# Performance work log

Hardware: AMD Instinct MI355X
Metric: run time of the kernel (lower is better)

The kernel has to match this reference:

```python
import jax, jax.numpy as jnp
import numpy as np

D_MODEL = 1024
BULK_DIM = 10          # int(log2(d_model))
ADS_RADIUS = 1.0
B, N = 4, 2048


def setup_inputs() -> dict:
    key = jax.random.key(0)
    k1, k2 = jax.random.split(key, 2)
    boundary_tokens = jax.random.normal(k1, (B, N, D_MODEL), dtype=jnp.float32)
    W_b2b = jax.random.normal(k2, (D_MODEL, D_MODEL * BULK_DIM), dtype=jnp.float32) / np.sqrt(D_MODEL).astype(np.float32)
    b_b2b = jnp.zeros((D_MODEL * BULK_DIM,), dtype=jnp.float32)
    return {"boundary_tokens": boundary_tokens, "W_b2b": W_b2b, "b_b2b": b_b2b}


def _fast_marching(bulk_coords, ads_radius):
    # bulk_coords: (B, N, K, D). Sequential eikonal-style sweep through the
    # bulk depth z = 1..K; AdS warp factor L/z attenuates the front update
    # deeper into the bulk. Returns geodesics with the same shape.
    cz = jnp.moveaxis(bulk_coords, 2, 0)                 # (K, B, N, D)
    z = jnp.arange(1, bulk_coords.shape[2] + 1, dtype=bulk_coords.dtype)
    factors = ads_radius / z                             # (K,)

    def step(g, inp):
        c, f = inp
        g_new = g + f * (c - g)
        return g_new, g_new

    _, geos = jax.lax.scan(step, cz[0], (cz, factors))   # (K, B, N, D)
    return jnp.moveaxis(geos, 0, 2)                      # (B, N, K, D)


def reference(boundary_tokens, W_b2b, b_b2b):
    Bb, Nn, D = boundary_tokens.shape
    # boundary -> bulk linear projection, reshaped to (B, N, bulk_dim, D)
    bulk_coords = (boundary_tokens @ W_b2b + b_b2b).reshape(Bb, Nn, BULK_DIM, D)
    geodesics = _fast_marching(bulk_coords, ADS_RADIUS)  # (B, N, K, D)
    bulk_features = geodesics.mean(axis=2)               # (B, N, D)
    return bulk_features
```

## Files before the change

### kernel.cpp

```cpp
#include <hip/hip_runtime.h>
#include <stdint.h>


static constexpr float FW[10] = {
    0.2928968253968254f, 0.1928968253968254f, 0.1428968253968254f,
    0.1095634920634921f, 0.0845634920634921f, 0.0645634920634921f,
    0.0478968253968254f, 0.0336111111111111f, 0.0211111111111111f,
    0.0100000000000000f};

typedef __attribute__((ext_vector_type(8))) short short8;
typedef __attribute__((ext_vector_type(4))) float floatx4;
typedef __attribute__((ext_vector_type(16))) float floatx16;

__device__ inline unsigned int bf16pack2(float hi, float lo) {
    unsigned int uh = __float_as_uint(hi) + 0x8000u;
    unsigned int ul = __float_as_uint(lo) + 0x8000u;
    return __builtin_amdgcn_perm(uh, ul, 0x07060302u);
}

#define LDS_AS(p) ((__attribute__((address_space(3))) unsigned int*)(p))
#define GLB_AS(p) ((const __attribute__((address_space(1))) unsigned int*)(p))

__global__ __launch_bounds__(256) void prep(const float* __restrict__ W,
                                            const float* __restrict__ tokens,
                                            const float* __restrict__ b,
                                            unsigned short* __restrict__ Wt,
                                            float* __restrict__ beff,
                                            uint4* __restrict__ Ab,
                                            int do_cvt) {
    __shared__ float T[32 * 65];
    const int t = threadIdx.x;
    const int bid = blockIdx.x;

    if (bid < 512) {
        const int n0 = (bid & 15) * 64;
        const int k0 = (bid >> 4) * 32;
#pragma unroll
        for (int s = 0; s < 2; ++s) {
            int slot = s * 256 + t;
            int r = slot >> 4;
            int c4 = (slot & 15) * 4;
            const float4* src = (const float4*)(W + (size_t)(k0 + r) * 10240 + n0 + c4);
            float4 acc = {0.f, 0.f, 0.f, 0.f};
#pragma unroll
            for (int j = 0; j < 10; ++j) {
                float4 v = src[j * 256];
                acc.x += FW[j] * v.x; acc.y += FW[j] * v.y;
                acc.z += FW[j] * v.z; acc.w += FW[j] * v.w;
            }
            T[r * 65 + c4 + 0] = acc.x;
            T[r * 65 + c4 + 1] = acc.y;
            T[r * 65 + c4 + 2] = acc.z;
            T[r * 65 + c4 + 3] = acc.w;
        }
        __syncthreads();
#pragma unroll
        for (int s = 0; s < 2; ++s) {
            int slot = s * 256 + t;
            int nl = slot >> 3;
            int k4 = (slot & 7) * 4;
            float f0 = T[(k4 + 0) * 65 + nl];
            float f1 = T[(k4 + 1) * 65 + nl];
            float f2 = T[(k4 + 2) * 65 + nl];
            float f3 = T[(k4 + 3) * 65 + nl];
            uint2 p;
            p.x = bf16pack2(f1, f0);
            p.y = bf16pack2(f3, f2);
            *(uint2*)(Wt + (size_t)(n0 + nl) * 1024 + k0 + k4) = p;
        }
        return;
    }
    if (bid == 512) {
        const float4* src = (const float4*)b + t;
        float4 acc = {0.f, 0.f, 0.f, 0.f};
#pragma unroll
        for (int j = 0; j < 10; ++j) {
            float4 v = src[j * 256];
            acc.x += FW[j] * v.x; acc.y += FW[j] * v.y;
            acc.z += FW[j] * v.z; acc.w += FW[j] * v.w;
        }
        ((float4*)beff)[t] = acc;
        return;
    }
    if (do_cvt) {
        size_t i = (size_t)(bid - 513) * 256 + t;
        const float4* src = (const float4*)tokens + i * 2;
        float4 a0 = src[0], a1 = src[1];
        uint4 p;
        p.x = bf16pack2(a0.y, a0.x);
        p.y = bf16pack2(a0.w, a0.z);
        p.z = bf16pack2(a1.y, a1.x);
        p.w = bf16pack2(a1.w, a1.z);
        Ab[i] = p;
    }
}

__global__ __launch_bounds__(256) void gemm32(const unsigned short* __restrict__ Ab,
                                              const unsigned short* __restrict__ Wt,
                                              const float* __restrict__ beff,
                                              float* __restrict__ C) {
    __shared__ __align__(16) unsigned char As[4][8192];
    __shared__ __align__(16) unsigned char Bs[4][8192];

    const int t = threadIdx.x;
    const int lane = t & 63;
    const int w = t >> 6;
    const int l31 = lane & 31;
    const int khalf = lane >> 5;
    const int wm = (w & 1) * 64;
    const int wn = (w >> 1) * 64;
    const int bm = blockIdx.x * 128;
    const int bn = blockIdx.y * 128;

    floatx16 acc[2][2];
#pragma unroll
    for (int i = 0; i < 2; ++i)
#pragma unroll
        for (int j = 0; j < 2; ++j)
#pragma unroll
            for (int r = 0; r < 16; ++r) acc[i][j][r] = 0.f;

    const char* Abase = (const char*)Ab + (size_t)bm * 2048;
    const char* Bbase = (const char*)Wt + (size_t)bn * 2048;

    int sm[2], sc[2];
#pragma unroll
    for (int i = 0; i < 2; ++i) {
        int s = (w * 2 + i) * 64 + lane;
        int pair = s >> 3;
        int q = (s & 7) ^ (pair & 7);
        sm[i] = pair * 2 + (q & 1);
        sc[i] = q >> 1;
    }

#define STAGE(KT)                                                                     \
    {                                                                                 \
        const size_t koff = (size_t)(KT) * 64;                                        \
        unsigned char* Ad = As[(KT) & 3];                                             \
        unsigned char* Bd = Bs[(KT) & 3];                                             \
        _Pragma("unroll") for (int i = 0; i < 2; ++i) {                               \
            int I = w * 2 + i;                                                        \
            __builtin_amdgcn_global_load_lds(                                         \
                GLB_AS(Abase + (size_t)sm[i] * 2048 + koff + sc[i] * 16),             \
                LDS_AS(Ad + I * 1024), 16, 0, 0);                                     \
            __builtin_amdgcn_global_load_lds(                                         \
                GLB_AS(Bbase + (size_t)sm[i] * 2048 + koff + sc[i] * 16),             \
                LDS_AS(Bd + I * 1024), 16, 0, 0);                                     \
        }                                                                             \
    }

    STAGE(0)
    STAGE(1)
    STAGE(2)

#pragma unroll
    for (int kt = 0; kt < 32; ++kt) {
        if (kt < 30)
            asm volatile("s_waitcnt vmcnt(8)" ::: "memory");
        else if (kt == 30)
            asm volatile("s_waitcnt vmcnt(4)" ::: "memory");
        else
            asm volatile("s_waitcnt vmcnt(0)" ::: "memory");
        __builtin_amdgcn_s_barrier();
        __builtin_amdgcn_sched_barrier(0);

        if (kt < 29) STAGE(kt + 3)
        __builtin_amdgcn_sched_barrier(0);

        const unsigned char* Acur = As[kt & 3];
        const unsigned char* Bcur = Bs[kt & 3];
#pragma unroll
        for (int kk = 0; kk < 2; ++kk) {
            int f = kk * 2 + khalf;
            short8 af[2], bf[2];
#pragma unroll
            for (int tm = 0; tm < 2; ++tm) {
                int m = wm + tm * 32 + l31;
                int slot = (m >> 1) * 8 + ((2 * f + (m & 1)) ^ ((m >> 1) & 7));
                af[tm] = *(const short8*)(Acur + slot * 16);
            }
#pragma unroll
            for (int tn = 0; tn < 2; ++tn) {
                int n = wn + tn * 32 + l31;
                int slot = (n >> 1) * 8 + ((2 * f + (n & 1)) ^ ((n >> 1) & 7));
                bf[tn] = *(const short8*)(Bcur + slot * 16);
            }
#pragma unroll
            for (int tm = 0; tm < 2; ++tm)
#pragma unroll
                for (int tn = 0; tn < 2; ++tn)
                    acc[tm][tn] = __builtin_amdgcn_mfma_f32_32x32x16_bf16(
                        af[tm], bf[tn], acc[tm][tn], 0, 0, 0);
        }
        __builtin_amdgcn_sched_barrier(0);
    }
#undef STAGE

#pragma unroll
    for (int tn = 0; tn < 2; ++tn) {
        int col = bn + wn + tn * 32 + l31;
        float bias = beff[col];
#pragma unroll
        for (int tm = 0; tm < 2; ++tm) {
            int rbase = bm + wm + tm * 32 + 4 * khalf;
#pragma unroll
            for (int r = 0; r < 16; ++r) {
                int row = rbase + (r & 3) + 8 * (r >> 2);
                C[(size_t)row * 1024 + col] = acc[tm][tn][r] + bias;
            }
        }
    }
}

__global__ __launch_bounds__(256) void gemm_fb(const float* __restrict__ A,
                                               const unsigned short* __restrict__ Wt,
                                               const float* __restrict__ beff,
                                               float* __restrict__ C) {
    __shared__ __align__(16) unsigned short Asl[128 * 72];
    __shared__ __align__(16) unsigned char Bsl[16384];

    const int t = threadIdx.x;
    const int lane = t & 63;
    const int w = t >> 6;
    const int quad = lane >> 4;
    const int l15 = lane & 15;
    const int wm = (w & 1) * 64;
    const int wn = (w >> 1) * 64;
    const int bm = blockIdx.y * 128;
    const int bn = blockIdx.x * 128;

    floatx4 acc[4][4];
#pragma unroll
    for (int i = 0; i < 4; ++i)
#pragma unroll
        for (int j = 0; j < 4; ++j) acc[i][j] = (floatx4){0.f, 0.f, 0.f, 0.f};

    const int ar = t >> 4;
    const int ac4 = (t & 15) * 4;
    const float* Abase = A + (size_t)(bm + ar) * 1024 + ac4;
    const char* WtB = (const char*)Wt;

    for (int k0 = 0; k0 < 1024; k0 += 64) {
#pragma unroll
        for (int i = 0; i < 4; ++i) {
            int I = w * 4 + i;
            int slot = I * 64 + lane;
            int nl = slot >> 3;
            int c = (slot & 7) ^ (nl & 7);
            const char* g = WtB + (size_t)(bn + nl) * 2048 + k0 * 2 + c * 16;
            __builtin_amdgcn_global_load_lds(GLB_AS(g), LDS_AS(Bsl + I * 1024), 16, 0, 0);
        }
        float4 av[8];
#pragma unroll
        for (int s = 0; s < 8; ++s)
            av[s] = *(const float4*)(Abase + (size_t)(s * 16) * 1024 + k0);
#pragma unroll
        for (int s = 0; s < 8; ++s) {
            uint2 p;
            p.x = bf16pack2(av[s].y, av[s].x);
            p.y = bf16pack2(av[s].w, av[s].z);
            *(uint2*)((char*)Asl + (size_t)(s * 16 + ar) * 144 + ac4 * 2) = p;
        }
        __syncthreads();
#pragma unroll
        for (int kk = 0; kk < 2; ++kk) {
            short8 af[4], bf[4];
#pragma unroll
            for (int tm = 0; tm < 4; ++tm) {
                int m = wm + tm * 16 + l15;
                af[tm] = *(const short8*)((const char*)Asl + (size_t)m * 144 + kk * 64 + quad * 16);
            }
#pragma unroll
            for (int tn = 0; tn < 4; ++tn) {
                int n = wn + tn * 16 + l15;
                int c = kk * 4 + quad;
                int slot = n * 8 + (c ^ (n & 7));
                bf[tn] = *(const short8*)(Bsl + slot * 16);
            }
#pragma unroll
            for (int tm = 0; tm < 4; ++tm)
#pragma unroll
                for (int tn = 0; tn < 4; ++tn)
                    acc[tm][tn] = __builtin_amdgcn_mfma_f32_16x16x32_bf16(
                        af[tm], bf[tn], acc[tm][tn], 0, 0, 0);
        }
        __syncthreads();
    }
#pragma unroll
    for (int tn = 0; tn < 4; ++tn) {
        int col = bn + wn + tn * 16 + l15;
        float bias = beff[col];
#pragma unroll
        for (int tm = 0; tm < 4; ++tm) {
            int row0 = bm + wm + tm * 16 + quad * 4;
#pragma unroll
            for (int r = 0; r < 4; ++r)
                C[(size_t)(row0 + r) * 1024 + col] = acc[tm][tn][r] + bias;
        }
    }
}

extern "C" void kernel_launch(void* const* d_in, const int* in_sizes, int n_in,
                              void* d_out, int out_size, void* d_ws, size_t ws_size,
                              hipStream_t stream) {
    const float* tokens = (const float*)d_in[0];
    const float* W      = (const float*)d_in[1];
    const float* b      = (const float*)d_in[2];
    float* out = (float*)d_out;

    unsigned short* Wt = (unsigned short*)d_ws;
    float* beff = (float*)((char*)d_ws + 2097152);
    unsigned short* Ab = (unsigned short*)((char*)d_ws + 2101248);

    const int big_ws = ws_size >= 2101248 + (size_t)8192 * 1024 * 2;

    if (big_ws) {
        prep<<<513 + 4096, 256, 0, stream>>>(W, tokens, b, Wt, beff, (uint4*)Ab, 1);
        gemm32<<<dim3(64, 8), 256, 0, stream>>>(Ab, Wt, beff, out);
    } else {
        prep<<<513, 256, 0, stream>>>(W, tokens, b, Wt, beff, (uint4*)Ab, 0);
        gemm_fb<<<dim3(8, 64), 256, 0, stream>>>(tokens, Wt, beff, out);
    }
}
```

Before: 133.2 us.

## Use 8 waves per GEMM block with 32x64 per-wave tiles

Doubles the gemm32 block from 4 to 8 wavefronts, so each wave computes a 32x64 sub-tile instead of 64x64 and issues one A and one B global-to-LDS load per stage instead of two. The wait counts are adjusted to match the smaller number of loads in flight per thread. The aim is more waves available to hide latency and less register pressure per wave. The cost is lower MFMA reuse per wave, since each B fragment now feeds only one A fragment, which doubles B LDS reads relative to compute.

```diff
diff --git a/kernel.cpp b/kernel.cpp
--- a/kernel.cpp
+++ b/kernel.cpp
@@ -95,7 +95,7 @@
     }
 }
 
-__global__ __launch_bounds__(256) void gemm32(const unsigned short* __restrict__ Ab,
+__global__ __launch_bounds__(512) void gemm32(const unsigned short* __restrict__ Ab,
                                               const unsigned short* __restrict__ Wt,
                                               const float* __restrict__ beff,
                                               float* __restrict__ C) {
@@ -107,46 +107,36 @@
     const int w = t >> 6;
     const int l31 = lane & 31;
     const int khalf = lane >> 5;
-    const int wm = (w & 1) * 64;
-    const int wn = (w >> 1) * 64;
+    const int wm = (w & 3) * 32;
+    const int wn = (w >> 2) * 64;
     const int bm = blockIdx.x * 128;
     const int bn = blockIdx.y * 128;
 
-    floatx16 acc[2][2];
-#pragma unroll
-    for (int i = 0; i < 2; ++i)
-#pragma unroll
-        for (int j = 0; j < 2; ++j)
-#pragma unroll
-            for (int r = 0; r < 16; ++r) acc[i][j][r] = 0.f;
+    floatx16 acc[2];
+#pragma unroll
+    for (int j = 0; j < 2; ++j)
+#pragma unroll
+        for (int r = 0; r < 16; ++r) acc[j][r] = 0.f;
 
     const char* Abase = (const char*)Ab + (size_t)bm * 2048;
     const char* Bbase = (const char*)Wt + (size_t)bn * 2048;
 
-    int sm[2], sc[2];
-#pragma unroll
-    for (int i = 0; i < 2; ++i) {
-        int s = (w * 2 + i) * 64 + lane;
-        int pair = s >> 3;
-        int q = (s & 7) ^ (pair & 7);
-        sm[i] = pair * 2 + (q & 1);
-        sc[i] = q >> 1;
-    }
+    const int pair = t >> 3;
+    const int q = (t & 7) ^ (pair & 7);
+    const int sm = pair * 2 + (q & 1);
+    const int sc = q >> 1;
 
 #define STAGE(KT)                                                                     \
     {                                                                                 \
         const size_t koff = (size_t)(KT) * 64;                                        \
         unsigned char* Ad = As[(KT) & 3];                                             \
         unsigned char* Bd = Bs[(KT) & 3];                                             \
-        _Pragma("unroll") for (int i = 0; i < 2; ++i) {                               \
-            int I = w * 2 + i;                                                        \
-            __builtin_amdgcn_global_load_lds(                                         \
-                GLB_AS(Abase + (size_t)sm[i] * 2048 + koff + sc[i] * 16),             \
-                LDS_AS(Ad + I * 1024), 16, 0, 0);                                     \
-            __builtin_amdgcn_global_load_lds(                                         \
-                GLB_AS(Bbase + (size_t)sm[i] * 2048 + koff + sc[i] * 16),             \
-                LDS_AS(Bd + I * 1024), 16, 0, 0);                                     \
-        }                                                                             \
+        __builtin_amdgcn_global_load_lds(                                             \
+            GLB_AS(Abase + (size_t)sm * 2048 + koff + sc * 16),                       \
+            LDS_AS(Ad + w * 1024), 16, 0, 0);                                         \
+        __builtin_amdgcn_global_load_lds(                                             \
+            GLB_AS(Bbase + (size_t)sm * 2048 + koff + sc * 16),                       \
+            LDS_AS(Bd + w * 1024), 16, 0, 0);                                         \
     }
 
     STAGE(0)
@@ -156,9 +146,9 @@
 #pragma unroll
     for (int kt = 0; kt < 32; ++kt) {
         if (kt < 30)
-            asm volatile("s_waitcnt vmcnt(8)" ::: "memory");
+            asm volatile("s_waitcnt vmcnt(4)" ::: "memory");
         else if (kt == 30)
-            asm volatile("s_waitcnt vmcnt(4)" ::: "memory");
+            asm volatile("s_waitcnt vmcnt(2)" ::: "memory");
         else
             asm volatile("s_waitcnt vmcnt(0)" ::: "memory");
         __builtin_amdgcn_s_barrier();
@@ -172,12 +162,11 @@
 #pragma unroll
         for (int kk = 0; kk < 2; ++kk) {
             int f = kk * 2 + khalf;
-            short8 af[2], bf[2];
-#pragma unroll
-            for (int tm = 0; tm < 2; ++tm) {
-                int m = wm + tm * 32 + l31;
+            short8 af, bf[2];
+            {
+                int m = wm + l31;
                 int slot = (m >> 1) * 8 + ((2 * f + (m & 1)) ^ ((m >> 1) & 7));
-                af[tm] = *(const short8*)(Acur + slot * 16);
+                af = *(const short8*)(Acur + slot * 16);
             }
 #pragma unroll
             for (int tn = 0; tn < 2; ++tn) {
@@ -186,11 +175,9 @@
                 bf[tn] = *(const short8*)(Bcur + slot * 16);
             }
 #pragma unroll
-            for (int tm = 0; tm < 2; ++tm)
-#pragma unroll
-                for (int tn = 0; tn < 2; ++tn)
-                    acc[tm][tn] = __builtin_amdgcn_mfma_f32_32x32x16_bf16(
-                        af[tm], bf[tn], acc[tm][tn], 0, 0, 0);
+            for (int tn = 0; tn < 2; ++tn)
+                acc[tn] = __builtin_amdgcn_mfma_f32_32x32x16_bf16(
+                    af, bf[tn], acc[tn], 0, 0, 0);
         }
         __builtin_amdgcn_sched_barrier(0);
     }
@@ -200,14 +187,11 @@
     for (int tn = 0; tn < 2; ++tn) {
         int col = bn + wn + tn * 32 + l31;
         float bias = beff[col];
-#pragma unroll
-        for (int tm = 0; tm < 2; ++tm) {
-            int rbase = bm + wm + tm * 32 + 4 * khalf;
-#pragma unroll
-            for (int r = 0; r < 16; ++r) {
-                int row = rbase + (r & 3) + 8 * (r >> 2);
-                C[(size_t)row * 1024 + col] = acc[tm][tn][r] + bias;
-            }
+        int rbase = bm + wm + 4 * khalf;
+#pragma unroll
+        for (int r = 0; r < 16; ++r) {
+            int row = rbase + (r & 3) + 8 * (r >> 2);
+            C[(size_t)row * 1024 + col] = acc[tn][r] + bias;
         }
     }
 }
@@ -316,7 +300,7 @@
 
     if (big_ws) {
         prep<<<513 + 4096, 256, 0, stream>>>(W, tokens, b, Wt, beff, (uint4*)Ab, 1);
-        gemm32<<<dim3(64, 8), 256, 0, stream>>>(Ab, Wt, beff, out);
+        gemm32<<<dim3(64, 8), 512, 0, stream>>>(Ab, Wt, beff, out);
     } else {
         prep<<<513, 256, 0, stream>>>(W, tokens, b, Wt, beff, (uint4*)Ab, 0);
         gemm_fb<<<dim3(8, 64), 256, 0, stream>>>(tokens, Wt, beff, out);
```

After: 131.5 us. About the same (-1.3%).
